# Performance work log

Measured on AMD Instinct MI355X. Metric: run time of the kernel, lower is better.

Reference implementation:

```python
import jax, jax.numpy as jnp
import numpy as np
from jax import lax

N_TRACES = 128
TRACE_LEN = 32          # uniform trace length -> seq_len
INPUT_DIM = 64
HIDDEN_DIM = 128
BATCH = N_TRACES * TRACE_LEN  # 4096 events = batch_size


def setup_inputs() -> dict:
    key = jax.random.key(0)
    ks = jax.random.split(key, 12)
    s = 1.0 / np.sqrt(HIDDEN_DIM)
    u = lambda k, shape: jax.random.uniform(k, shape, jnp.float32, -s, s)
    return {
        "input": jax.random.normal(ks[0], (BATCH, INPUT_DIM), jnp.float32),
        # layer 0 LSTM params (gate order i,f,g,o as in torch)
        "W_ih0": u(ks[1], (4 * HIDDEN_DIM, INPUT_DIM)),
        "W_hh0": u(ks[2], (4 * HIDDEN_DIM, HIDDEN_DIM)),
        "b_ih0": u(ks[3], (4 * HIDDEN_DIM,)),
        "b_hh0": u(ks[4], (4 * HIDDEN_DIM,)),
        # layer 1 LSTM params
        "W_ih1": u(ks[5], (4 * HIDDEN_DIM, HIDDEN_DIM)),
        "W_hh1": u(ks[6], (4 * HIDDEN_DIM, HIDDEN_DIM)),
        "b_ih1": u(ks[7], (4 * HIDDEN_DIM,)),
        "b_hh1": u(ks[8], (4 * HIDDEN_DIM,)),
        # final linear: hidden -> 1
        "W_lin": u(ks[9], (1, HIDDEN_DIM)),
        "b_lin": u(ks[10], (1,)),
    }


def _lstm_layer(xs, W_ih, W_hh, b_ih, b_hh):
    # xs: [T, B, D_in] time-major. Returns hidden stream [T, B, H].
    H = W_hh.shape[1]
    B = xs.shape[1]
    # precompute input projection for all timesteps
    x_proj = jnp.einsum('tbd,gd->tbg', xs, W_ih) + b_ih + b_hh  # [T,B,4H]

    def step(carry, xp):
        h, c = carry
        gates = xp + h @ W_hh.T                # [B,4H]
        i, f, g, o = jnp.split(gates, 4, axis=-1)
        i = jax.nn.sigmoid(i)
        f = jax.nn.sigmoid(f)
        g = jnp.tanh(g)
        o = jax.nn.sigmoid(o)
        c = f * c + i * g
        h = o * jnp.tanh(c)
        return (h, c), h

    h0 = jnp.zeros((B, H), xs.dtype)
    _, hs = lax.scan(step, (h0, h0), x_proj)
    return hs


def _forward(input, W_ih0, W_hh0, b_ih0, b_hh0, W_ih1, W_hh1, b_ih1, b_hh1, W_lin, b_lin):
    L, D = TRACE_LEN, INPUT_DIM
    # Prefix scatter: event k of a trace gets the padded prefix events[0..k].
    x_tr = input.reshape(N_TRACES, L, D)                       # [Ntr, L, D]
    causal = (jnp.arange(L)[None, :] <= jnp.arange(L)[:, None])  # [k, j] mask j<=k
    padded = x_tr[:, None, :, :] * causal[None, :, :, None].astype(input.dtype)  # [Ntr,L(k),L(j),D]
    padded = padded.reshape(BATCH, L, D)                       # batch-first padded sequences

    xs = jnp.transpose(padded, (1, 0, 2))                      # [L, B, D] time-major
    h1 = _lstm_layer(xs, W_ih0, W_hh0, b_ih0, b_hh0)           # [L, B, H]
    h2 = _lstm_layer(h1, W_ih1, W_hh1, b_ih1, b_hh1)           # [L, B, H]

    out = jnp.einsum('tbh,oh->tbo', h2, W_lin) + b_lin         # [L, B, 1]
    # last valid timestep gather: lengths[i]-1 = (i mod L)
    lens_m1 = jnp.tile(jnp.arange(L), N_TRACES)                # [B]
    y_pred = out[lens_m1, jnp.arange(BATCH), 0]                # [B]
    return y_pred


def reference(input, W_ih0, W_hh0, b_ih0, b_hh0, W_ih1, W_hh1, b_ih1, b_hh1, W_lin, b_lin):
    return _forward(input, W_ih0, W_hh0, b_ih0, b_hh0, W_ih1, W_hh1, b_ih1, b_hh1, W_lin, b_lin)
```

## Files before the change

### kernel.cpp

```cpp
#include <hip/hip_runtime.h>

#define N_TRACES 128
#define TLEN 32
#define IN_DIM 64
#define HID 128
#define G4 (4 * HID)
#define BATCH (N_TRACES * TLEN)

typedef float f32x4 __attribute__((ext_vector_type(4)));
typedef __bf16 bf16x8 __attribute__((ext_vector_type(8)));


__device__ __forceinline__ float fast_sigmoid(float x) {
    return 1.0f / (1.0f + __expf(-x));
}
__device__ __forceinline__ float fast_tanh(float x) {
    return 1.0f - 2.0f / (__expf(2.0f * x) + 1.0f);
}
__device__ __forceinline__ float quad_reduce(float x) {
    x += __int_as_float(__builtin_amdgcn_update_dpp(
        0, __float_as_int(x), 0xB1 , 0xF, 0xF, true));
    x += __int_as_float(__builtin_amdgcn_update_dpp(
        0, __float_as_int(x), 0x4E , 0xF, 0xF, true));
    return x;
}

__device__ __forceinline__ void load_w(const float* __restrict__ W, int u, int s,
                                       float (&w)[4][32]) {
    #pragma unroll
    for (int i = 0; i < 4; ++i) {
        const float* wr = W + (size_t)(u + 128 * i) * HID + 32 * s;
        #pragma unroll
        for (int j = 0; j < 8; ++j) {
            float4 v = *(const float4*)(wr + 4 * j);
            w[i][4 * j + 0] = v.x; w[i][4 * j + 1] = v.y;
            w[i][4 * j + 2] = v.z; w[i][4 * j + 3] = v.w;
        }
    }
    #pragma unroll
    for (int i = 0; i < 4; ++i)
        #pragma unroll
        for (int j = 0; j < 32; ++j)
            asm volatile("" : "+v"(w[i][j]));
}

__device__ __forceinline__ void matvec_acc(const float (&w)[4][32],
                                           const float* hb, float (&acc)[4]) {
    #pragma unroll
    for (int j = 0; j < 8; ++j) {
        float4 v = *(const float4*)(hb + 4 * j);
        float hx[4] = {v.x, v.y, v.z, v.w};
        #pragma unroll
        for (int e = 0; e < 4; ++e) {
            #pragma unroll
            for (int i = 0; i < 4; ++i)
                acc[i] = fmaf(w[i][4 * j + e], hx[e], acc[i]);
        }
    }
}


__device__ __forceinline__ void load_wfrag(const float* __restrict__ W, int u, int q,
                                           bf16x8 (&bh)[4][4], bf16x8 (&bl)[4][4])
{
    #pragma unroll
    for (int gi = 0; gi < 4; ++gi) {
        const float* wr = W + (size_t)(u + 128 * gi) * HID + 8 * q;
        #pragma unroll
        for (int kc = 0; kc < 4; ++kc) {
            float4 v0 = *(const float4*)(wr + 32 * kc);
            float4 v1 = *(const float4*)(wr + 32 * kc + 4);
            float f0[4] = {v0.x, v0.y, v0.z, v0.w};
            float f1[4] = {v1.x, v1.y, v1.z, v1.w};
            bf16x8 h, l;
            #pragma unroll
            for (int e = 0; e < 4; ++e) {
                __bf16 t0 = (__bf16)f0[e];
                h[e] = t0; l[e] = (__bf16)(f0[e] - (float)t0);
                __bf16 t1 = (__bf16)f1[e];
                h[4 + e] = t1; l[4 + e] = (__bf16)(f1[e] - (float)t1);
            }
            bh[gi][kc] = h; bl[gi][kc] = l;
        }
    }
}

__device__ __forceinline__ void mm3(const bf16x8 (&ah)[4], const bf16x8 (&al)[4],
                                    const bf16x8 (&bh)[4][4], const bf16x8 (&bl)[4][4],
                                    f32x4 (&acc)[4])
{
    #pragma unroll
    for (int gi = 0; gi < 4; ++gi) {
        #pragma unroll
        for (int kc = 0; kc < 4; ++kc) {
            acc[gi] = __builtin_amdgcn_mfma_f32_16x16x32_bf16(ah[kc], bh[gi][kc], acc[gi], 0, 0, 0);
            acc[gi] = __builtin_amdgcn_mfma_f32_16x16x32_bf16(al[kc], bh[gi][kc], acc[gi], 0, 0, 0);
            acc[gi] = __builtin_amdgcn_mfma_f32_16x16x32_bf16(ah[kc], bl[gi][kc], acc[gi], 0, 0, 0);
        }
    }
}


template <int K>
__global__ __launch_bounds__(256) void gemm_bt(
    const float* __restrict__ A,
    const float* __restrict__ W,
    const float* __restrict__ b1,
    const float* __restrict__ b2,
    float* __restrict__ out,
    int Nld)
{
    constexpr int LD = 68;
    __shared__ float At[K][LD];
    __shared__ float Wt[K][LD];

    const int tid = threadIdx.x;
    const int m0 = blockIdx.x * 64;
    const int n0 = blockIdx.y * 64;

    const int rot = tid & 3;
    #pragma unroll
    for (int j = 0; j < K / 16; ++j) {
        const int e = 4 * (tid + 256 * j);
        const int row = e / K;
        const int k = e % K;
        float4 va = *(const float4*)(A + (size_t)(m0 + row) * K + k);
        float4 vw = *(const float4*)(W + (size_t)(n0 + row) * K + k);
        float fa[4] = {va.x, va.y, va.z, va.w};
        float fw[4] = {vw.x, vw.y, vw.z, vw.w};
        #pragma unroll
        for (int ii = 0; ii < 4; ++ii) {
            const int i = (ii + rot) & 3;
            At[k + i][row] = fa[i];
            Wt[k + i][row] = fw[i];
        }
    }
    __syncthreads();

    const int tx = tid & 15;
    const int ty = tid >> 4;
    float acc[4][4] = {};

    #pragma unroll 4
    for (int k = 0; k < K; ++k) {
        float4 a = *(const float4*)&At[k][ty * 4];
        float4 w = *(const float4*)&Wt[k][tx * 4];
        acc[0][0] = fmaf(a.x, w.x, acc[0][0]); acc[0][1] = fmaf(a.x, w.y, acc[0][1]);
        acc[0][2] = fmaf(a.x, w.z, acc[0][2]); acc[0][3] = fmaf(a.x, w.w, acc[0][3]);
        acc[1][0] = fmaf(a.y, w.x, acc[1][0]); acc[1][1] = fmaf(a.y, w.y, acc[1][1]);
        acc[1][2] = fmaf(a.y, w.z, acc[1][2]); acc[1][3] = fmaf(a.y, w.w, acc[1][3]);
        acc[2][0] = fmaf(a.z, w.x, acc[2][0]); acc[2][1] = fmaf(a.z, w.y, acc[2][1]);
        acc[2][2] = fmaf(a.z, w.z, acc[2][2]); acc[2][3] = fmaf(a.z, w.w, acc[2][3]);
        acc[3][0] = fmaf(a.w, w.x, acc[3][0]); acc[3][1] = fmaf(a.w, w.y, acc[3][1]);
        acc[3][2] = fmaf(a.w, w.z, acc[3][2]); acc[3][3] = fmaf(a.w, w.w, acc[3][3]);
    }

    float bb[4];
    #pragma unroll
    for (int j = 0; j < 4; ++j) {
        const int n = n0 + tx * 4 + j;
        bb[j] = b1[n] + b2[n];
    }
    #pragma unroll
    for (int i = 0; i < 4; ++i) {
        const int m = m0 + ty * 4 + i;
        float4 v;
        v.x = acc[i][0] + bb[0]; v.y = acc[i][1] + bb[1];
        v.z = acc[i][2] + bb[2]; v.w = acc[i][3] + bb[3];
        *(float4*)(out + (size_t)m * Nld + n0 + tx * 4) = v;
    }
}


__global__ __launch_bounds__(512) void fused_trace(
    const float* __restrict__ xproj0,
    const float* __restrict__ Whh0,
    const float* __restrict__ Wih1,
    const float* __restrict__ bih1,
    const float* __restrict__ bhh1,
    const float* __restrict__ Whh1,
    const float* __restrict__ Wlin,
    const float* __restrict__ blin,
    float* __restrict__ y)
{
    const int trace = blockIdx.x;
    const int tid = threadIdx.x;
    const int u = tid >> 2;
    const int s = tid & 3;
    const int pu = u + 4 * (u >> 5);

    __shared__ float hs[TLEN][140];
    __shared__ float xp[TLEN * G4];

    float w[4][32];

    const float* xpb = xproj0 + (size_t)trace * TLEN * G4;
    #pragma unroll
    for (int j = 0; j < 8; ++j) {
        const int f4 = j * 512 + tid;
        float4 v = *(const float4*)(xpb + 4 * f4);
        *(float4*)(&xp[4 * f4]) = v;
    }
    load_w(Whh0, u, s, w);
    __syncthreads();

    float xg[4], xgn[4];
    #pragma unroll
    for (int i = 0; i < 4; ++i) xg[i] = xp[128 * i + u];
    #pragma unroll
    for (int i = 0; i < 4; ++i) xgn[i] = xp[G4 + 128 * i + u];

    float c = 0.0f;
    if (s == 0) {
        const float iv = fast_sigmoid(xg[0]);
        const float fv = fast_sigmoid(xg[1]);
        const float gv = fast_tanh(xg[2]);
        const float ov = fast_sigmoid(xg[3]);
        c = fv * c + iv * gv;
        hs[0][pu] = ov * fast_tanh(c);
    }
    __syncthreads();

    #pragma unroll 1
    for (int t = 1; t < TLEN; ++t) {
        #pragma unroll
        for (int i = 0; i < 4; ++i) xg[i] = xgn[i];

        float acc[4] = {0.f, 0.f, 0.f, 0.f};
        matvec_acc(w, &hs[t - 1][36 * s], acc);
        #pragma unroll
        for (int i = 0; i < 4; ++i) acc[i] = quad_reduce(acc[i]);

        if (s == 0) {
            const float iv = fast_sigmoid(acc[0] + xg[0]);
            const float fv = fast_sigmoid(acc[1] + xg[1]);
            const float gv = fast_tanh(acc[2] + xg[2]);
            const float ov = fast_sigmoid(acc[3] + xg[3]);
            c = fv * c + iv * gv;
            hs[t][pu] = ov * fast_tanh(c);
        }
        if (t < TLEN - 1) {
            #pragma unroll
            for (int i = 0; i < 4; ++i)
                xgn[i] = xp[(t + 1) * G4 + 128 * i + u];
        }
        __syncthreads();
    }

    {
        const int w8 = tid >> 6;
        const int lane = tid & 63;
        const int cl = lane & 15;
        const int q = lane >> 4;
        const int um = 16 * w8 + cl;

        bf16x8 Bh[4][4], Bl[4][4];
        load_wfrag(Wih1, um, q, Bh, Bl);
        float bim[4];
        #pragma unroll
        for (int gi = 0; gi < 4; ++gi)
            bim[gi] = bih1[um + 128 * gi] + bhh1[um + 128 * gi];

        #pragma unroll
        for (int mt = 0; mt < 2; ++mt) {
            bf16x8 ah[4], al[4];
            #pragma unroll
            for (int kc = 0; kc < 4; ++kc) {
                const float* ph = &hs[16 * mt + cl][36 * kc + 8 * q];
                float4 v0 = *(const float4*)(ph);
                float4 v1 = *(const float4*)(ph + 4);
                float f0[4] = {v0.x, v0.y, v0.z, v0.w};
                float f1[4] = {v1.x, v1.y, v1.z, v1.w};
                bf16x8 hh, ll;
                #pragma unroll
                for (int e = 0; e < 4; ++e) {
                    __bf16 t0 = (__bf16)f0[e];
                    hh[e] = t0; ll[e] = (__bf16)(f0[e] - (float)t0);
                    __bf16 t1 = (__bf16)f1[e];
                    hh[4 + e] = t1; ll[4 + e] = (__bf16)(f1[e] - (float)t1);
                }
                ah[kc] = hh; al[kc] = ll;
            }
            f32x4 acc[4];
            #pragma unroll
            for (int gi = 0; gi < 4; ++gi) acc[gi] = (f32x4){0.f, 0.f, 0.f, 0.f};
            mm3(ah, al, Bh, Bl, acc);
            #pragma unroll
            for (int gi = 0; gi < 4; ++gi)
                #pragma unroll
                for (int r = 0; r < 4; ++r)
                    xp[(16 * mt + 4 * q + r) * G4 + 128 * gi + um] = acc[gi][r] + bim[gi];
        }
    }
    __syncthreads();

    load_w(Whh1, u, s, w);
    #pragma unroll
    for (int i = 0; i < 4; ++i) xg[i] = xp[128 * i + u];
    #pragma unroll
    for (int i = 0; i < 4; ++i) xgn[i] = xp[G4 + 128 * i + u];

    c = 0.0f;
    if (s == 0) {
        const float iv = fast_sigmoid(xg[0]);
        const float fv = fast_sigmoid(xg[1]);
        const float gv = fast_tanh(xg[2]);
        const float ov = fast_sigmoid(xg[3]);
        c = fv * c + iv * gv;
        hs[0][pu] = ov * fast_tanh(c);
    }
    __syncthreads();

    #pragma unroll 1
    for (int t = 1; t < TLEN; ++t) {
        #pragma unroll
        for (int i = 0; i < 4; ++i) xg[i] = xgn[i];

        float acc[4] = {0.f, 0.f, 0.f, 0.f};
        matvec_acc(w, &hs[t - 1][36 * s], acc);
        #pragma unroll
        for (int i = 0; i < 4; ++i) acc[i] = quad_reduce(acc[i]);

        if (s == 0) {
            const float iv = fast_sigmoid(acc[0] + xg[0]);
            const float fv = fast_sigmoid(acc[1] + xg[1]);
            const float gv = fast_tanh(acc[2] + xg[2]);
            const float ov = fast_sigmoid(acc[3] + xg[3]);
            c = fv * c + iv * gv;
            hs[t][pu] = ov * fast_tanh(c);
        }
        if (t < TLEN - 1) {
            #pragma unroll
            for (int i = 0; i < 4; ++i)
                xgn[i] = xp[(t + 1) * G4 + 128 * i + u];
        }
        __syncthreads();
    }

    if (tid < 128) {
        const int tq = tid >> 2;
        const int sq = tid & 3;
        float wl[32];
        #pragma unroll
        for (int j = 0; j < 8; ++j) {
            float4 v = *(const float4*)(Wlin + 32 * sq + 4 * j);
            wl[4 * j + 0] = v.x; wl[4 * j + 1] = v.y;
            wl[4 * j + 2] = v.z; wl[4 * j + 3] = v.w;
        }
        const float* hb = &hs[tq][36 * sq];
        float a = 0.f;
        #pragma unroll
        for (int j = 0; j < 8; ++j) {
            float4 v = *(const float4*)(hb + 4 * j);
            a = fmaf(v.x, wl[4 * j + 0], a);
            a = fmaf(v.y, wl[4 * j + 1], a);
            a = fmaf(v.z, wl[4 * j + 2], a);
            a = fmaf(v.w, wl[4 * j + 3], a);
        }
        a = quad_reduce(a);
        if (sq == 0) y[trace * TLEN + tq] = a + blin[0];
    }
}


extern "C" void kernel_launch(void* const* d_in, const int* in_sizes, int n_in,
                              void* d_out, int out_size, void* d_ws, size_t ws_size,
                              hipStream_t stream) {
    const float* input = (const float*)d_in[0];
    const float* W_ih0 = (const float*)d_in[1];
    const float* W_hh0 = (const float*)d_in[2];
    const float* b_ih0 = (const float*)d_in[3];
    const float* b_hh0 = (const float*)d_in[4];
    const float* W_ih1 = (const float*)d_in[5];
    const float* W_hh1 = (const float*)d_in[6];
    const float* b_ih1 = (const float*)d_in[7];
    const float* b_hh1 = (const float*)d_in[8];
    const float* W_lin = (const float*)d_in[9];
    const float* b_lin = (const float*)d_in[10];
    float* out = (float*)d_out;

    float* xproj0 = (float*)d_ws;

    dim3 ggrid(BATCH / 64, G4 / 64);

    gemm_bt<IN_DIM><<<ggrid, 256, 0, stream>>>(input, W_ih0, b_ih0, b_hh0, xproj0, G4);
    fused_trace<<<N_TRACES, 512, 0, stream>>>(xproj0, W_hh0, W_ih1, b_ih1, b_hh1,
                                              W_hh1, W_lin, b_lin, out);
}
```

Before: 153.4 us.

## Fuse layer-0 input projection into the per-trace kernel using split-bf16 MFMA

Drops the separate FP32 GEMM kernel that wrote the layer-0 input projection to workspace. Each trace block now computes its own 32x512 projection from the input with three-term split-bf16 MFMAs, the same way it already handles the layer-1 projection. This removes a kernel launch and a global-memory round trip for the projection buffer. In exchange, every block reloads and converts the W_ih0 fragments, and register pressure rises in the prologue.

New measurement: 148.9 us, median of 2. 1.03x faster.

```diff
diff --git a/kernel.cpp b/kernel.cpp
--- a/kernel.cpp
+++ b/kernel.cpp
@@ -60,120 +60,26 @@
 }
 
 
-__device__ __forceinline__ void load_wfrag(const float* __restrict__ W, int u, int q,
-                                           bf16x8 (&bh)[4][4], bf16x8 (&bl)[4][4])
-{
-    #pragma unroll
-    for (int gi = 0; gi < 4; ++gi) {
-        const float* wr = W + (size_t)(u + 128 * gi) * HID + 8 * q;
-        #pragma unroll
-        for (int kc = 0; kc < 4; ++kc) {
-            float4 v0 = *(const float4*)(wr + 32 * kc);
-            float4 v1 = *(const float4*)(wr + 32 * kc + 4);
-            float f0[4] = {v0.x, v0.y, v0.z, v0.w};
-            float f1[4] = {v1.x, v1.y, v1.z, v1.w};
-            bf16x8 h, l;
-            #pragma unroll
-            for (int e = 0; e < 4; ++e) {
-                __bf16 t0 = (__bf16)f0[e];
-                h[e] = t0; l[e] = (__bf16)(f0[e] - (float)t0);
-                __bf16 t1 = (__bf16)f1[e];
-                h[4 + e] = t1; l[4 + e] = (__bf16)(f1[e] - (float)t1);
-            }
-            bh[gi][kc] = h; bl[gi][kc] = l;
-        }
-    }
-}
-
-__device__ __forceinline__ void mm3(const bf16x8 (&ah)[4], const bf16x8 (&al)[4],
-                                    const bf16x8 (&bh)[4][4], const bf16x8 (&bl)[4][4],
-                                    f32x4 (&acc)[4])
-{
-    #pragma unroll
-    for (int gi = 0; gi < 4; ++gi) {
-        #pragma unroll
-        for (int kc = 0; kc < 4; ++kc) {
-            acc[gi] = __builtin_amdgcn_mfma_f32_16x16x32_bf16(ah[kc], bh[gi][kc], acc[gi], 0, 0, 0);
-            acc[gi] = __builtin_amdgcn_mfma_f32_16x16x32_bf16(al[kc], bh[gi][kc], acc[gi], 0, 0, 0);
-            acc[gi] = __builtin_amdgcn_mfma_f32_16x16x32_bf16(ah[kc], bl[gi][kc], acc[gi], 0, 0, 0);
-        }
-    }
-}
-
-
-template <int K>
-__global__ __launch_bounds__(256) void gemm_bt(
-    const float* __restrict__ A,
-    const float* __restrict__ W,
-    const float* __restrict__ b1,
-    const float* __restrict__ b2,
-    float* __restrict__ out,
-    int Nld)
-{
-    constexpr int LD = 68;
-    __shared__ float At[K][LD];
-    __shared__ float Wt[K][LD];
-
-    const int tid = threadIdx.x;
-    const int m0 = blockIdx.x * 64;
-    const int n0 = blockIdx.y * 64;
-
-    const int rot = tid & 3;
-    #pragma unroll
-    for (int j = 0; j < K / 16; ++j) {
-        const int e = 4 * (tid + 256 * j);
-        const int row = e / K;
-        const int k = e % K;
-        float4 va = *(const float4*)(A + (size_t)(m0 + row) * K + k);
-        float4 vw = *(const float4*)(W + (size_t)(n0 + row) * K + k);
-        float fa[4] = {va.x, va.y, va.z, va.w};
-        float fw[4] = {vw.x, vw.y, vw.z, vw.w};
-        #pragma unroll
-        for (int ii = 0; ii < 4; ++ii) {
-            const int i = (ii + rot) & 3;
-            At[k + i][row] = fa[i];
-            Wt[k + i][row] = fw[i];
-        }
-    }
-    __syncthreads();
-
-    const int tx = tid & 15;
-    const int ty = tid >> 4;
-    float acc[4][4] = {};
-
-    #pragma unroll 4
-    for (int k = 0; k < K; ++k) {
-        float4 a = *(const float4*)&At[k][ty * 4];
-        float4 w = *(const float4*)&Wt[k][tx * 4];
-        acc[0][0] = fmaf(a.x, w.x, acc[0][0]); acc[0][1] = fmaf(a.x, w.y, acc[0][1]);
-        acc[0][2] = fmaf(a.x, w.z, acc[0][2]); acc[0][3] = fmaf(a.x, w.w, acc[0][3]);
-        acc[1][0] = fmaf(a.y, w.x, acc[1][0]); acc[1][1] = fmaf(a.y, w.y, acc[1][1]);
-        acc[1][2] = fmaf(a.y, w.z, acc[1][2]); acc[1][3] = fmaf(a.y, w.w, acc[1][3]);
-        acc[2][0] = fmaf(a.z, w.x, acc[2][0]); acc[2][1] = fmaf(a.z, w.y, acc[2][1]);
-        acc[2][2] = fmaf(a.z, w.z, acc[2][2]); acc[2][3] = fmaf(a.z, w.w, acc[2][3]);
-        acc[3][0] = fmaf(a.w, w.x, acc[3][0]); acc[3][1] = fmaf(a.w, w.y, acc[3][1]);
-        acc[3][2] = fmaf(a.w, w.z, acc[3][2]); acc[3][3] = fmaf(a.w, w.w, acc[3][3]);
-    }
-
-    float bb[4];
-    #pragma unroll
-    for (int j = 0; j < 4; ++j) {
-        const int n = n0 + tx * 4 + j;
-        bb[j] = b1[n] + b2[n];
-    }
-    #pragma unroll
-    for (int i = 0; i < 4; ++i) {
-        const int m = m0 + ty * 4 + i;
-        float4 v;
-        v.x = acc[i][0] + bb[0]; v.y = acc[i][1] + bb[1];
-        v.z = acc[i][2] + bb[2]; v.w = acc[i][3] + bb[3];
-        *(float4*)(out + (size_t)m * Nld + n0 + tx * 4) = v;
+__device__ __forceinline__ void split8(const float* p, bf16x8& h, bf16x8& l) {
+    float4 v0 = *(const float4*)(p);
+    float4 v1 = *(const float4*)(p + 4);
+    float f0[4] = {v0.x, v0.y, v0.z, v0.w};
+    float f1[4] = {v1.x, v1.y, v1.z, v1.w};
+    #pragma unroll
+    for (int e = 0; e < 4; ++e) {
+        __bf16 t0 = (__bf16)f0[e];
+        h[e] = t0; l[e] = (__bf16)(f0[e] - (float)t0);
+        __bf16 t1 = (__bf16)f1[e];
+        h[4 + e] = t1; l[4 + e] = (__bf16)(f1[e] - (float)t1);
     }
 }
 
 
 __global__ __launch_bounds__(512) void fused_trace(
-    const float* __restrict__ xproj0,
+    const float* __restrict__ input,
+    const float* __restrict__ Wih0,
+    const float* __restrict__ bih0,
+    const float* __restrict__ bhh0,
     const float* __restrict__ Whh0,
     const float* __restrict__ Wih1,
     const float* __restrict__ bih1,
@@ -194,12 +100,51 @@
 
     float w[4][32];
 
-    const float* xpb = xproj0 + (size_t)trace * TLEN * G4;
-    #pragma unroll
-    for (int j = 0; j < 8; ++j) {
-        const int f4 = j * 512 + tid;
-        float4 v = *(const float4*)(xpb + 4 * f4);
-        *(float4*)(&xp[4 * f4]) = v;
+    {
+        const int w8 = tid >> 6;
+        const int lane = tid & 63;
+        const int cl = lane & 15;
+        const int q = lane >> 4;
+        const int um = 16 * w8 + cl;
+
+        bf16x8 Bh[4][2], Bl[4][2];
+        #pragma unroll
+        for (int gi = 0; gi < 4; ++gi)
+            #pragma unroll
+            for (int kc = 0; kc < 2; ++kc)
+                split8(Wih0 + (size_t)(um + 128 * gi) * IN_DIM + 32 * kc + 8 * q,
+                       Bh[gi][kc], Bl[gi][kc]);
+        float bb[4];
+        #pragma unroll
+        for (int gi = 0; gi < 4; ++gi)
+            bb[gi] = bih0[um + 128 * gi] + bhh0[um + 128 * gi];
+
+        #pragma unroll
+        for (int mt = 0; mt < 2; ++mt) {
+            bf16x8 ah[2], al[2];
+            const float* pr = input + (size_t)(trace * TLEN + 16 * mt + cl) * IN_DIM;
+            #pragma unroll
+            for (int kc = 0; kc < 2; ++kc)
+                split8(pr + 32 * kc + 8 * q, ah[kc], al[kc]);
+
+            f32x4 acc[4];
+            #pragma unroll
+            for (int gi = 0; gi < 4; ++gi) acc[gi] = (f32x4){0.f, 0.f, 0.f, 0.f};
+            #pragma unroll
+            for (int gi = 0; gi < 4; ++gi) {
+                #pragma unroll
+                for (int kc = 0; kc < 2; ++kc) {
+                    acc[gi] = __builtin_amdgcn_mfma_f32_16x16x32_bf16(ah[kc], Bh[gi][kc], acc[gi], 0, 0, 0);
+                    acc[gi] = __builtin_amdgcn_mfma_f32_16x16x32_bf16(al[kc], Bh[gi][kc], acc[gi], 0, 0, 0);
+                    acc[gi] = __builtin_amdgcn_mfma_f32_16x16x32_bf16(ah[kc], Bl[gi][kc], acc[gi], 0, 0, 0);
+                }
+            }
+            #pragma unroll
+            for (int gi = 0; gi < 4; ++gi)
+                #pragma unroll
+                for (int r = 0; r < 4; ++r)
+                    xp[(16 * mt + 4 * q + r) * G4 + 128 * gi + um] = acc[gi][r] + bb[gi];
+        }
     }
     load_w(Whh0, u, s, w);
     __syncthreads();
@@ -255,7 +200,12 @@
         const int um = 16 * w8 + cl;
 
         bf16x8 Bh[4][4], Bl[4][4];
-        load_wfrag(Wih1, um, q, Bh, Bl);
+        #pragma unroll
+        for (int gi = 0; gi < 4; ++gi)
+            #pragma unroll
+            for (int kc = 0; kc < 4; ++kc)
+                split8(Wih1 + (size_t)(um + 128 * gi) * HID + 32 * kc + 8 * q,
+                       Bh[gi][kc], Bl[gi][kc]);
         float bim[4];
         #pragma unroll
         for (int gi = 0; gi < 4; ++gi)
@@ -265,26 +215,21 @@
         for (int mt = 0; mt < 2; ++mt) {
             bf16x8 ah[4], al[4];
             #pragma unroll
-            for (int kc = 0; kc < 4; ++kc) {
-                const float* ph = &hs[16 * mt + cl][36 * kc + 8 * q];
-                float4 v0 = *(const float4*)(ph);
-                float4 v1 = *(const float4*)(ph + 4);
-                float f0[4] = {v0.x, v0.y, v0.z, v0.w};
-                float f1[4] = {v1.x, v1.y, v1.z, v1.w};
-                bf16x8 hh, ll;
+            for (int kc = 0; kc < 4; ++kc)
+                split8(&hs[16 * mt + cl][36 * kc + 8 * q], ah[kc], al[kc]);
+
+            f32x4 acc[4];
+            #pragma unroll
+            for (int gi = 0; gi < 4; ++gi) acc[gi] = (f32x4){0.f, 0.f, 0.f, 0.f};
+            #pragma unroll
+            for (int gi = 0; gi < 4; ++gi) {
                 #pragma unroll
-                for (int e = 0; e < 4; ++e) {
-                    __bf16 t0 = (__bf16)f0[e];
-                    hh[e] = t0; ll[e] = (__bf16)(f0[e] - (float)t0);
-                    __bf16 t1 = (__bf16)f1[e];
-                    hh[4 + e] = t1; ll[4 + e] = (__bf16)(f1[e] - (float)t1);
+                for (int kc = 0; kc < 4; ++kc) {
+                    acc[gi] = __builtin_amdgcn_mfma_f32_16x16x32_bf16(ah[kc], Bh[gi][kc], acc[gi], 0, 0, 0);
+                    acc[gi] = __builtin_amdgcn_mfma_f32_16x16x32_bf16(al[kc], Bh[gi][kc], acc[gi], 0, 0, 0);
+                    acc[gi] = __builtin_amdgcn_mfma_f32_16x16x32_bf16(ah[kc], Bl[gi][kc], acc[gi], 0, 0, 0);
                 }
-                ah[kc] = hh; al[kc] = ll;
             }
-            f32x4 acc[4];
-            #pragma unroll
-            for (int gi = 0; gi < 4; ++gi) acc[gi] = (f32x4){0.f, 0.f, 0.f, 0.f};
-            mm3(ah, al, Bh, Bl, acc);
             #pragma unroll
             for (int gi = 0; gi < 4; ++gi)
                 #pragma unroll
@@ -379,11 +324,7 @@
     const float* b_lin = (const float*)d_in[10];
     float* out = (float*)d_out;
 
-    float* xproj0 = (float*)d_ws;
-
-    dim3 ggrid(BATCH / 64, G4 / 64);
-
-    gemm_bt<IN_DIM><<<ggrid, 256, 0, stream>>>(input, W_ih0, b_ih0, b_hh0, xproj0, G4);
-    fused_trace<<<N_TRACES, 512, 0, stream>>>(xproj0, W_hh0, W_ih1, b_ih1, b_hh1,
+    fused_trace<<<N_TRACES, 512, 0, stream>>>(input, W_ih0, b_ih0, b_hh0,
+                                              W_hh0, W_ih1, b_ih1, b_hh1,
                                               W_hh1, W_lin, b_lin, out);
 }
```
